# Optimization experiments

Measured on AMD Instinct MI355X. Metric: run time of the kernel, lower is better.

The kernel has to match this reference:

```python
import jax, jax.numpy as jnp
import numpy as np

B, DIN, DK, DV, H, DOUT = 16384, 2048, 2048, 2048, 16, 512
dk, dv = DK // H, DV // H  # 128, 128

def setup_inputs() -> dict:
    key = jax.random.key(0)
    ks = jax.random.split(key, 10)
    s_in = 1.0 / np.sqrt(DIN)
    s_v = 1.0 / np.sqrt(DV)
    s_2in = 1.0 / np.sqrt(2 * DIN)
    return {
        "x": jax.random.normal(ks[0], (B, DIN), jnp.float32),
        "Wq": jax.random.normal(ks[1], (DIN, DK), jnp.float32) * s_in,
        "Wk": jax.random.normal(ks[2], (DIN, DK), jnp.float32) * s_in,
        "Wv": jax.random.normal(ks[3], (DIN, DV), jnp.float32) * s_in,
        "Wo": jax.random.normal(ks[4], (DV, DIN), jnp.float32) * s_v,
        "bo": jax.random.normal(ks[5], (DIN,), jnp.float32) * s_v,
        "Wg": jax.random.normal(ks[6], (2 * DIN, DIN), jnp.float32) * s_2in,
        "bg": jax.random.normal(ks[7], (DIN,), jnp.float32) * s_2in,
        "Wout": jax.random.normal(ks[8], (DIN, DOUT), jnp.float32) * s_in,
        "bout": jax.random.normal(ks[9], (DOUT,), jnp.float32) * s_in,
    }

def _feat(t):
    # kernel feature map: relu(x) + 1e-4
    return jax.nn.relu(t) + 1e-4

def reference(x, Wq, Wk, Wv, Wo, bo, Wg, bg, Wout, bout):
    b = x.shape[0]
    q = _feat((x @ Wq).reshape(b, H, dk))
    k = _feat((x @ Wk).reshape(b, H, dk))
    v = (x @ Wv).reshape(b, H, dv)
    # linear attention: aggregate over batch (acts as sequence)
    kv = jnp.einsum('bhd,bhe->hde', k, v)            # [H, dk, dv]
    z = 1.0 / (jnp.einsum('bhd,hd->bh', q, k.sum(axis=0)) + 1e-6)  # [B, H]
    att = jnp.einsum('bhd,hde->bhe', q, kv) * z[..., None]         # [B, H, dv]
    att = att.reshape(b, DV)
    out_proj = att @ Wo + bo
    gate = jax.nn.sigmoid(jnp.concatenate([out_proj, x], axis=-1) @ Wg + bg)
    out = gate * out_proj + (1.0 - gate) * x
    return out @ Wout + bout
```

## Files before the change

kernel.cpp:

```cpp
#include <hip/hip_runtime.h>
#include <hip/hip_bf16.h>
#include <math.h>

typedef __bf16 bf16_t;
typedef __attribute__((ext_vector_type(8))) __bf16 bf16x8;
typedef __attribute__((ext_vector_type(4))) __bf16 bf16x4;
typedef __attribute__((ext_vector_type(4))) float f32x4;
typedef __attribute__((ext_vector_type(16))) float f32x16;

#define DEVI __device__ __forceinline__

constexpr int B_SZ = 16384, DIN = 2048, DK = 2048, DV = 2048, NH = 16, DOUT = 512;

DEVI void load_lds16(const void* gptr, void* lptr) {
  __builtin_amdgcn_global_load_lds(
      (const __attribute__((address_space(1))) unsigned int*)gptr,
      (__attribute__((address_space(3))) unsigned int*)lptr,
      16, 0, 0);
}

template <int EPI>
__global__ __launch_bounds__(256) void gemm_bt(
    const bf16_t* __restrict__ A, int lda, long aZ,
    const bf16_t* __restrict__ Bt, int ldb, long bZ,
    void* __restrict__ Cv, int ldc, long cZ, int K,
    const float* __restrict__ aux1,
    const float* __restrict__ aux2) {
  __shared__ __align__(16) bf16_t As[2][128 * 32];
  __shared__ __align__(16) bf16_t Bs[2][128 * 32];
  const int tid = threadIdx.x;
  const int bn = blockIdx.x, bm = blockIdx.y, bz = blockIdx.z;
  const int lane = tid & 63, w = tid >> 6;
  const int wm = (w & 1) * 64, wn = (w >> 1) * 64;
  const int lm = lane & 31, lh = lane >> 5;

  const bf16_t* Ab = A + (long)bm * 128 * lda + (long)bz * aZ;
  const bf16_t* Bb = Bt + (long)bn * 128 * ldb + (long)bz * bZ;

  const int srow = tid >> 2;
  const int scol = ((tid & 3) ^ ((tid >> 3) & 3)) * 8;

  f32x16 acc[2][2] = {};

  for (int k0 = 0; k0 < K; k0 += 64) {
#pragma unroll
    for (int kk = 0; kk < 2; ++kk) {
#pragma unroll
      for (int it = 0; it < 2; ++it) {
        load_lds16(Ab + (long)(srow + it * 64) * lda + k0 + kk * 32 + scol,
                   &As[kk][it * 2048 + tid * 8]);
        load_lds16(Bb + (long)(srow + it * 64) * ldb + k0 + kk * 32 + scol,
                   &Bs[kk][it * 2048 + tid * 8]);
      }
    }
    __syncthreads();
#pragma unroll
    for (int s = 0; s < 4; ++s) {
      const int kk = s >> 1;
      const int cg = (s & 1) * 2 + lh;
      bf16x8 af[2], bfr[2];
#pragma unroll
      for (int i = 0; i < 2; ++i) {
        const int R = wm + i * 32 + lm;
        af[i] = *(const bf16x8*)&As[kk][R * 32 + ((cg ^ ((R >> 1) & 3)) * 8)];
      }
#pragma unroll
      for (int j = 0; j < 2; ++j) {
        const int R = wn + j * 32 + lm;
        bfr[j] = *(const bf16x8*)&Bs[kk][R * 32 + ((cg ^ ((R >> 1) & 3)) * 8)];
      }
#pragma unroll
      for (int i = 0; i < 2; ++i)
#pragma unroll
        for (int j = 0; j < 2; ++j)
          acc[i][j] = __builtin_amdgcn_mfma_f32_32x32x16_bf16(af[i], bfr[j], acc[i][j], 0, 0, 0);
    }
    __syncthreads();
  }

#pragma unroll
  for (int i = 0; i < 2; ++i) {
#pragma unroll
    for (int j = 0; j < 2; ++j) {
      const int col = bn * 128 + wn + j * 32 + lm;
#pragma unroll
      for (int r = 0; r < 16; ++r) {
        const int row = bm * 128 + wm + i * 32 + (r & 3) + 8 * (r >> 2) + 4 * lh;
        const long cidx = (long)row * ldc + (long)bz * cZ + col;
        float val = acc[i][j][r];
        if (EPI == 0) {
          ((bf16_t*)Cv)[cidx] = (bf16_t)val;
        } else if (EPI == 1) {
          if (col < 4096) val = fmaxf(val, 0.f) + 1e-4f;
          ((bf16_t*)Cv)[cidx] = (bf16_t)val;
        } else if (EPI == 2) {
          val += aux1[col];
          ((bf16_t*)Cv)[cidx] = (bf16_t)val;
        } else if (EPI == 4) {
          const float g = 1.f / (1.f + __expf(-(val + aux1[col])));
          const float op = (float)A[(long)row * lda + col];
          const float xx = aux2[(long)row * DIN + col];
          ((bf16_t*)Cv)[cidx] = (bf16_t)(g * op + (1.f - g) * xx);
        } else if (EPI == 5) {
          ((float*)Cv)[cidx] = val + aux1[col];
        }
      }
    }
  }
}

__global__ __launch_bounds__(256) void cvt_x_kernel(const float* __restrict__ x,
                                                    bf16_t* __restrict__ cc) {
  const long i = ((long)blockIdx.x * 256 + threadIdx.x) * 4;
  const long row = i >> 11;
  const int col = (int)(i & 2047);
  const float4 f = *(const float4*)&x[i];
  bf16x4 o;
  o[0] = (bf16_t)f.x; o[1] = (bf16_t)f.y; o[2] = (bf16_t)f.z; o[3] = (bf16_t)f.w;
  *(bf16x4*)&cc[row * 4096 + 2048 + col] = o;
}

__global__ __launch_bounds__(256) void transpose_f32_bf16(const float* __restrict__ in,
                                                          bf16_t* __restrict__ out,
                                                          int R, int C) {
  __shared__ bf16_t tile[32][33];
  const int c0 = blockIdx.x * 32, r0 = blockIdx.y * 32;
  for (int i = threadIdx.y; i < 32; i += 8)
    tile[i][threadIdx.x] = (bf16_t)in[(long)(r0 + i) * C + c0 + threadIdx.x];
  __syncthreads();
  for (int i = threadIdx.y; i < 32; i += 8)
    out[(long)(c0 + i) * R + r0 + threadIdx.x] = tile[threadIdx.x][i];
}

__global__ __launch_bounds__(256) void ksum_kernel(const bf16_t* __restrict__ qkv,
                                                   float* __restrict__ ksum) {
  const int col = blockIdx.x * 256 + threadIdx.x;
  const int r0 = blockIdx.y * 256;
  const bf16_t* k = qkv + 2048;
  float s = 0.f;
  for (int r = 0; r < 256; ++r) s += (float)k[(long)(r0 + r) * 6144 + col];
  atomicAdd(&ksum[col], s);
}

__global__ __launch_bounds__(256) void kv_kernel(const bf16_t* __restrict__ qkv,
                                                 float* __restrict__ P) {
  const int h = blockIdx.x, sp = blockIdx.y;
  const int t = threadIdx.x;
  __shared__ __align__(16) bf16_t kS[64 * 128];
  __shared__ __align__(16) bf16_t vS[64 * 128];
  const int d0 = (t >> 4) * 8, e0 = (t & 15) * 8;
  const int srow = t >> 4, scol = (t & 15) * 8;
  float acc[8][8] = {};
  const bf16_t* kp = qkv + 2048 + h * 128;
  const bf16_t* vp = qkv + 4096 + h * 128;
  const long base = (long)sp * 512 * 6144;
  for (int c0 = 0; c0 < 512; c0 += 64) {
#pragma unroll
    for (int it = 0; it < 4; ++it) {
      load_lds16(kp + base + (long)(c0 + it * 16 + srow) * 6144 + scol, &kS[it * 2048 + t * 8]);
      load_lds16(vp + base + (long)(c0 + it * 16 + srow) * 6144 + scol, &vS[it * 2048 + t * 8]);
    }
    __syncthreads();
    for (int bb = 0; bb < 64; ++bb) {
      const bf16x8 kk = *(const bf16x8*)&kS[bb * 128 + d0];
      const bf16x8 vv = *(const bf16x8*)&vS[bb * 128 + e0];
      float kf[8], vf[8];
#pragma unroll
      for (int r = 0; r < 8; ++r) { kf[r] = (float)kk[r]; vf[r] = (float)vv[r]; }
#pragma unroll
      for (int a = 0; a < 8; ++a)
#pragma unroll
        for (int b2 = 0; b2 < 8; ++b2) acc[a][b2] += kf[a] * vf[b2];
    }
    __syncthreads();
  }
  float* Ph = P + (long)h * 16384;
#pragma unroll
  for (int a = 0; a < 8; ++a)
#pragma unroll
    for (int b2 = 0; b2 < 8; ++b2)
      atomicAdd(&Ph[(d0 + a) * 128 + e0 + b2], acc[a][b2]);
}

__global__ __launch_bounds__(256) void cvt_bf(const float* __restrict__ P,
                                              bf16_t* __restrict__ o, int n) {
  const int i = blockIdx.x * 256 + threadIdx.x;
  if (i < n) o[i] = (bf16_t)P[i];
}

__global__ __launch_bounds__(256) void z_kernel(bf16_t* __restrict__ qkv,
                                                const float* __restrict__ ksum) {
  __shared__ float ks[2048];
  const int t = threadIdx.x;
  for (int i = t; i < 2048; i += 256) ks[i] = ksum[i];
  __syncthreads();
  const int b = blockIdx.x * 16 + (t >> 4);
  const int h = t & 15;
  bf16_t* qr = qkv + (long)b * 6144 + h * 128;
  bf16x8 qq[16];
  float s = 0.f;
#pragma unroll
  for (int i = 0; i < 16; ++i) {
    qq[i] = *(const bf16x8*)&qr[i * 8];
#pragma unroll
    for (int r = 0; r < 8; ++r) s += (float)qq[i][r] * ks[h * 128 + i * 8 + r];
  }
  const float z = 1.f / (s + 1e-6f);
#pragma unroll
  for (int i = 0; i < 16; ++i) {
#pragma unroll
    for (int r = 0; r < 8; ++r) qq[i][r] = (bf16_t)((float)qq[i][r] * z);
    *(bf16x8*)&qr[i * 8] = qq[i];
  }
}

extern "C" void kernel_launch(void* const* d_in, const int* in_sizes, int n_in,
                              void* d_out, int out_size, void* d_ws, size_t ws_size,
                              hipStream_t stream) {
  const float* x    = (const float*)d_in[0];
  const float* Wq   = (const float*)d_in[1];
  const float* Wk   = (const float*)d_in[2];
  const float* Wv   = (const float*)d_in[3];
  const float* Wo   = (const float*)d_in[4];
  const float* bo   = (const float*)d_in[5];
  const float* Wg   = (const float*)d_in[6];
  const float* bg   = (const float*)d_in[7];
  const float* Wout = (const float*)d_in[8];
  const float* bout = (const float*)d_in[9];

  char* ws = (char*)d_ws;
  size_t off = 0;
  auto alloc = [&](size_t bytes) -> void* {
    void* p = ws + off;
    off += (bytes + 255) & ~(size_t)255;
    return p;
  };
  bf16_t* concat = (bf16_t*)alloc((size_t)B_SZ * 4096 * 2);
  bf16_t* qkv    = (bf16_t*)alloc((size_t)B_SZ * 6144 * 2);
  bf16_t* outb   = (bf16_t*)alloc((size_t)B_SZ * DIN * 2);
  bf16_t* WqkvT  = (bf16_t*)alloc((size_t)6144 * DIN * 2);
  bf16_t* WoT    = (bf16_t*)alloc((size_t)DIN * DV * 2);
  bf16_t* WgT    = (bf16_t*)alloc((size_t)DIN * 4096 * 2);
  bf16_t* WoutT  = (bf16_t*)alloc((size_t)DOUT * DIN * 2);
  float*  P      = (float*)alloc((size_t)NH * 128 * 128 * 4);
  bf16_t* kvbf   = (bf16_t*)alloc((size_t)NH * 128 * 128 * 2);
  bf16_t* G      = (bf16_t*)alloc((size_t)DIN * DK * 2);
  float*  ksum   = (float*)alloc((size_t)DK * 4);

  hipMemsetAsync(P, 0, (size_t)NH * 128 * 128 * 4, stream);
  hipMemsetAsync(ksum, 0, (size_t)DK * 4, stream);

  cvt_x_kernel<<<(B_SZ * DIN) / 1024, 256, 0, stream>>>(x, concat);

  const dim3 tb(32, 8);
  transpose_f32_bf16<<<dim3(64, 64), tb, 0, stream>>>(Wq, WqkvT, 2048, 2048);
  transpose_f32_bf16<<<dim3(64, 64), tb, 0, stream>>>(Wk, WqkvT + (size_t)2048 * 2048, 2048, 2048);
  transpose_f32_bf16<<<dim3(64, 64), tb, 0, stream>>>(Wv, WqkvT + (size_t)4096 * 2048, 2048, 2048);
  transpose_f32_bf16<<<dim3(64, 64), tb, 0, stream>>>(Wo, WoT, 2048, 2048);
  transpose_f32_bf16<<<dim3(64, 128), tb, 0, stream>>>(Wg, WgT, 4096, 2048);
  transpose_f32_bf16<<<dim3(16, 64), tb, 0, stream>>>(Wout, WoutT, 2048, 512);

  const bf16_t* xb = concat + 2048;

  gemm_bt<1><<<dim3(48, 128, 1), 256, 0, stream>>>(xb, 4096, 0, WqkvT, 2048, 0,
                                                   qkv, 6144, 0, 2048, nullptr, nullptr);

  ksum_kernel<<<dim3(8, 64), 256, 0, stream>>>(qkv, ksum);
  kv_kernel<<<dim3(16, 32), 256, 0, stream>>>(qkv, P);
  cvt_bf<<<1024, 256, 0, stream>>>(P, kvbf, NH * 128 * 128);
  z_kernel<<<B_SZ / 16, 256, 0, stream>>>(qkv, ksum);

  gemm_bt<0><<<dim3(1, 16, 16), 256, 0, stream>>>(WoT, 2048, 128, kvbf, 128, 16384,
                                                  G, 2048, 128, 128, nullptr, nullptr);

  gemm_bt<2><<<dim3(16, 128, 1), 256, 0, stream>>>(qkv, 6144, 0, G, 2048, 0,
                                                   concat, 4096, 0, 2048, bo, nullptr);

  gemm_bt<4><<<dim3(16, 128, 1), 256, 0, stream>>>(concat, 4096, 0, WgT, 4096, 0,
                                                   outb, 2048, 0, 4096, bg, x);

  gemm_bt<5><<<dim3(4, 128, 1), 256, 0, stream>>>(outb, 2048, 0, WoutT, 2048, 0,
                                                  d_out, 512, 0, 2048, bout, nullptr);
}
```

Measured before the change: 1.776 ms.

## Fuse prep kernels, simplify GEMM LDS addressing, raise GEMM occupancy hint

Merges the x-to-bf16 conversion and the six weight transposes into one prep kernel, so seven launches become one. Drops the XOR swizzle in the GEMM's LDS staging and reads, and replaces the per-iteration index math with precomputed base pointers and fixed offsets. Adds a min-blocks-per-CU hint of 4 to the GEMM's launch bounds. Without the swizzle the fragment reads from LDS may hit bank conflicts, and the occupancy hint may force register spills.

```diff
diff --git a/kernel.cpp b/kernel.cpp
--- a/kernel.cpp
+++ b/kernel.cpp
@@ -5,7 +5,6 @@
 typedef __bf16 bf16_t;
 typedef __attribute__((ext_vector_type(8))) __bf16 bf16x8;
 typedef __attribute__((ext_vector_type(4))) __bf16 bf16x4;
-typedef __attribute__((ext_vector_type(4))) float f32x4;
 typedef __attribute__((ext_vector_type(16))) float f32x16;
 
 #define DEVI __device__ __forceinline__
@@ -20,7 +19,7 @@
 }
 
 template <int EPI>
-__global__ __launch_bounds__(256) void gemm_bt(
+__global__ __launch_bounds__(256, 4) void gemm_bt(
     const bf16_t* __restrict__ A, int lda, long aZ,
     const bf16_t* __restrict__ Bt, int ldb, long bZ,
     void* __restrict__ Cv, int ldc, long cZ, int K,
@@ -34,46 +33,41 @@
   const int wm = (w & 1) * 64, wn = (w >> 1) * 64;
   const int lm = lane & 31, lh = lane >> 5;
 
-  const bf16_t* Ab = A + (long)bm * 128 * lda + (long)bz * aZ;
-  const bf16_t* Bb = Bt + (long)bn * 128 * ldb + (long)bz * bZ;
-
-  const int srow = tid >> 2;
-  const int scol = ((tid & 3) ^ ((tid >> 3) & 3)) * 8;
+  const bf16_t* __restrict__ Ab = A + (long)bm * 128 * lda + (long)bz * aZ;
+  const bf16_t* __restrict__ Bb = Bt + (long)bn * 128 * ldb + (long)bz * bZ;
+
+  const int srow = tid >> 2, scol = (tid & 3) * 8;
+  const long aRow = (long)srow * lda + scol;
+  const long bRow = (long)srow * ldb + scol;
+
+  const char* aBase = (const char*)As + (wm + lm) * 64 + lh * 16;
+  const char* bBase = (const char*)Bs + (wn + lm) * 64 + lh * 16;
 
   f32x16 acc[2][2] = {};
 
   for (int k0 = 0; k0 < K; k0 += 64) {
-#pragma unroll
-    for (int kk = 0; kk < 2; ++kk) {
-#pragma unroll
-      for (int it = 0; it < 2; ++it) {
-        load_lds16(Ab + (long)(srow + it * 64) * lda + k0 + kk * 32 + scol,
-                   &As[kk][it * 2048 + tid * 8]);
-        load_lds16(Bb + (long)(srow + it * 64) * ldb + k0 + kk * 32 + scol,
-                   &Bs[kk][it * 2048 + tid * 8]);
-      }
-    }
+    const bf16_t* ap = Ab + aRow + k0;
+    const bf16_t* bp = Bb + bRow + k0;
+    load_lds16(ap, &As[0][tid * 8]);
+    load_lds16(ap + (long)64 * lda, &As[0][2048 + tid * 8]);
+    load_lds16(ap + 32, &As[1][tid * 8]);
+    load_lds16(ap + (long)64 * lda + 32, &As[1][2048 + tid * 8]);
+    load_lds16(bp, &Bs[0][tid * 8]);
+    load_lds16(bp + (long)64 * ldb, &Bs[0][2048 + tid * 8]);
+    load_lds16(bp + 32, &Bs[1][tid * 8]);
+    load_lds16(bp + (long)64 * ldb + 32, &Bs[1][2048 + tid * 8]);
     __syncthreads();
 #pragma unroll
     for (int s = 0; s < 4; ++s) {
-      const int kk = s >> 1;
-      const int cg = (s & 1) * 2 + lh;
-      bf16x8 af[2], bfr[2];
-#pragma unroll
-      for (int i = 0; i < 2; ++i) {
-        const int R = wm + i * 32 + lm;
-        af[i] = *(const bf16x8*)&As[kk][R * 32 + ((cg ^ ((R >> 1) & 3)) * 8)];
-      }
-#pragma unroll
-      for (int j = 0; j < 2; ++j) {
-        const int R = wn + j * 32 + lm;
-        bfr[j] = *(const bf16x8*)&Bs[kk][R * 32 + ((cg ^ ((R >> 1) & 3)) * 8)];
-      }
-#pragma unroll
-      for (int i = 0; i < 2; ++i)
-#pragma unroll
-        for (int j = 0; j < 2; ++j)
-          acc[i][j] = __builtin_amdgcn_mfma_f32_32x32x16_bf16(af[i], bfr[j], acc[i][j], 0, 0, 0);
+      const int off = (s >> 1) * 8192 + (s & 1) * 32;
+      const bf16x8 af0 = *(const bf16x8*)(aBase + off);
+      const bf16x8 af1 = *(const bf16x8*)(aBase + off + 2048);
+      const bf16x8 bf0 = *(const bf16x8*)(bBase + off);
+      const bf16x8 bf1 = *(const bf16x8*)(bBase + off + 2048);
+      acc[0][0] = __builtin_amdgcn_mfma_f32_32x32x16_bf16(af0, bf0, acc[0][0], 0, 0, 0);
+      acc[0][1] = __builtin_amdgcn_mfma_f32_32x32x16_bf16(af0, bf1, acc[0][1], 0, 0, 0);
+      acc[1][0] = __builtin_amdgcn_mfma_f32_32x32x16_bf16(af1, bf0, acc[1][0], 0, 0, 0);
+      acc[1][1] = __builtin_amdgcn_mfma_f32_32x32x16_bf16(af1, bf1, acc[1][1], 0, 0, 0);
     }
     __syncthreads();
   }
@@ -109,27 +103,42 @@
   }
 }
 
-__global__ __launch_bounds__(256) void cvt_x_kernel(const float* __restrict__ x,
-                                                    bf16_t* __restrict__ cc) {
-  const long i = ((long)blockIdx.x * 256 + threadIdx.x) * 4;
-  const long row = i >> 11;
-  const int col = (int)(i & 2047);
-  const float4 f = *(const float4*)&x[i];
-  bf16x4 o;
-  o[0] = (bf16_t)f.x; o[1] = (bf16_t)f.y; o[2] = (bf16_t)f.z; o[3] = (bf16_t)f.w;
-  *(bf16x4*)&cc[row * 4096 + 2048 + col] = o;
-}
-
-__global__ __launch_bounds__(256) void transpose_f32_bf16(const float* __restrict__ in,
-                                                          bf16_t* __restrict__ out,
-                                                          int R, int C) {
+__global__ __launch_bounds__(256) void prep_kernel(
+    const float* __restrict__ x, const float* __restrict__ Wq,
+    const float* __restrict__ Wk, const float* __restrict__ Wv,
+    const float* __restrict__ Wo, const float* __restrict__ Wg,
+    const float* __restrict__ Wout, bf16_t* __restrict__ concat,
+    bf16_t* __restrict__ WqkvT, bf16_t* __restrict__ WoT,
+    bf16_t* __restrict__ WgT, bf16_t* __restrict__ WoutT) {
+  const int tid = threadIdx.x;
+  int b = blockIdx.x;
+  if (b < 32768) {
+    const long i = ((long)b * 256 + tid) * 4;
+    const long row = i >> 11;
+    const int col = (int)(i & 2047);
+    const float4 f = *(const float4*)&x[i];
+    bf16x4 o;
+    o[0] = (bf16_t)f.x; o[1] = (bf16_t)f.y; o[2] = (bf16_t)f.z; o[3] = (bf16_t)f.w;
+    *(bf16x4*)&concat[row * 4096 + 2048 + col] = o;
+    return;
+  }
+  b -= 32768;
+  const float* in; bf16_t* out; int R, C;
+  if (b < 4096)       { in = Wq;   out = WqkvT;                     R = 2048; C = 2048; }
+  else if (b < 8192)  { in = Wk;   out = WqkvT + (size_t)2048*2048; R = 2048; C = 2048; b -= 4096; }
+  else if (b < 12288) { in = Wv;   out = WqkvT + (size_t)4096*2048; R = 2048; C = 2048; b -= 8192; }
+  else if (b < 16384) { in = Wo;   out = WoT;                       R = 2048; C = 2048; b -= 12288; }
+  else if (b < 24576) { in = Wg;   out = WgT;                       R = 4096; C = 2048; b -= 16384; }
+  else                { in = Wout; out = WoutT;                     R = 2048; C = 512;  b -= 24576; }
+  const int CB = C / 32;
+  const int c0 = (b % CB) * 32, r0 = (b / CB) * 32;
   __shared__ bf16_t tile[32][33];
-  const int c0 = blockIdx.x * 32, r0 = blockIdx.y * 32;
-  for (int i = threadIdx.y; i < 32; i += 8)
-    tile[i][threadIdx.x] = (bf16_t)in[(long)(r0 + i) * C + c0 + threadIdx.x];
+  const int tx = tid & 31, ty = tid >> 5;
+  for (int i = ty; i < 32; i += 8)
+    tile[i][tx] = (bf16_t)in[(long)(r0 + i) * C + c0 + tx];
   __syncthreads();
-  for (int i = threadIdx.y; i < 32; i += 8)
-    out[(long)(c0 + i) * R + r0 + threadIdx.x] = tile[threadIdx.x][i];
+  for (int i = ty; i < 32; i += 8)
+    out[(long)(c0 + i) * R + r0 + tx] = tile[tx][i];
 }
 
 __global__ __launch_bounds__(256) void ksum_kernel(const bf16_t* __restrict__ qkv,
@@ -250,15 +259,8 @@
   hipMemsetAsync(P, 0, (size_t)NH * 128 * 128 * 4, stream);
   hipMemsetAsync(ksum, 0, (size_t)DK * 4, stream);
 
-  cvt_x_kernel<<<(B_SZ * DIN) / 1024, 256, 0, stream>>>(x, concat);
-
-  const dim3 tb(32, 8);
-  transpose_f32_bf16<<<dim3(64, 64), tb, 0, stream>>>(Wq, WqkvT, 2048, 2048);
-  transpose_f32_bf16<<<dim3(64, 64), tb, 0, stream>>>(Wk, WqkvT + (size_t)2048 * 2048, 2048, 2048);
-  transpose_f32_bf16<<<dim3(64, 64), tb, 0, stream>>>(Wv, WqkvT + (size_t)4096 * 2048, 2048, 2048);
-  transpose_f32_bf16<<<dim3(64, 64), tb, 0, stream>>>(Wo, WoT, 2048, 2048);
-  transpose_f32_bf16<<<dim3(64, 128), tb, 0, stream>>>(Wg, WgT, 4096, 2048);
-  transpose_f32_bf16<<<dim3(16, 64), tb, 0, stream>>>(Wout, WoutT, 2048, 512);
+  prep_kernel<<<32768 + 25600, 256, 0, stream>>>(x, Wq, Wk, Wv, Wo, Wg, Wout,
+                                                 concat, WqkvT, WoT, WgT, WoutT);
 
   const bf16_t* xb = concat + 2048;
 
```

Measured after the change: 1.729 ms. 2.7% less time.
